# Kernel tuning notes

Measured on AMD Instinct MI355X. Metric: run time of the kernel, lower is better.

The kernel has to match this reference:

```python
import jax, jax.numpy as jnp
import numpy as np

# Model dims (match init_kwargs)
DIM = 1024
EXPAND = 2
D_INNER = DIM * EXPAND          # 2048
D_STATE = 16
D_CONV = 4
DT_RANK = max(16, DIM // 16)    # 64
BATCH = 2
SEQ = 1024
EPS_RMS = 1e-6


def setup_inputs() -> dict:
    key = jax.random.key(0)
    ks = jax.random.split(key, 10)
    def nrm(k, shape, scale=0.02):
        return jax.random.normal(k, shape, jnp.float32) * scale
    x = jax.random.normal(ks[0], (BATCH, SEQ, DIM), jnp.float32)
    W_in = nrm(ks[1], (2 * D_INNER, DIM))                      # in_proj, no bias
    W_conv = nrm(ks[2], (D_INNER, D_CONV), 0.1)                # depthwise conv weight (squeezed)
    b_conv = nrm(ks[3], (D_INNER,), 0.01)
    W_x = nrm(ks[4], (DT_RANK + 2 * D_STATE, D_INNER))         # x_proj, no bias
    dt_std = DT_RANK ** -0.5 * 0.1
    W_dt = jax.random.uniform(ks[5], (D_INNER, DT_RANK), jnp.float32, -dt_std, dt_std)
    b_dt = jax.random.uniform(ks[6], (D_INNER,), jnp.float32, 1e-3, 0.1)
    # HiPPO-style A init: A = arange(1..d_state) + small noise, A_log = log(A)
    A = jnp.arange(1, D_STATE + 1, dtype=jnp.float32)[None, :] + 0.01 * jax.random.normal(ks[7], (D_INNER, D_STATE), jnp.float32)
    A_log = jnp.log(A + 1e-8)
    D = jnp.ones((D_INNER,), jnp.float32) * 0.1
    rms_w = jnp.ones((D_INNER,), jnp.float32)                  # RMSNorm weight
    W_out = nrm(ks[8], (DIM, D_INNER))                         # out_proj, no bias
    return dict(x=x, W_in=W_in, W_conv=W_conv, b_conv=b_conv, W_x=W_x,
                W_dt=W_dt, b_dt=b_dt, A_log=A_log, D=D, rms_w=rms_w, W_out=W_out)


def _ssm_forward(x, W_in, W_conv, b_conv, W_x, W_dt, b_dt, A_log, D, rms_w, W_out):
    b, s, _ = x.shape
    # input projection -> [b, s, 2*d_inner], split into x branch and gate z
    xz = jnp.einsum('bsd,ed->bse', x, W_in)
    x_in, z = jnp.split(xz, 2, axis=-1)
    # depthwise causal conv1d (torch pads d_conv-1 both sides then slices to seq_len == left pad)
    xpad = jnp.pad(x_in, ((0, 0), (D_CONV - 1, 0), (0, 0)))
    xc = b_conv
    for k in range(D_CONV):
        xc = xc + W_conv[:, k] * xpad[:, k:k + s, :]
    xc = jax.nn.silu(xc)                                       # [b, s, d_inner]
    # data-dependent SSM params
    dbl = jnp.einsum('bsd,ed->bse', xc, W_x)
    dt, Bm, Cm = jnp.split(dbl, [DT_RANK, DT_RANK + D_STATE], axis=-1)
    dt = jax.nn.softplus(jnp.einsum('bsr,dr->bsd', dt, W_dt) + b_dt) + 1e-4  # [b,s,d_inner]
    A = -jnp.exp(A_log)                                        # [d_inner, d_state]
    # discretize: dA = exp(clip(dt*A)), dB*u
    dA = jnp.exp(jnp.clip(dt[..., None] * A, -10.0, 10.0))     # [b,s,d,n]
    dBu = dt[..., None] * Bm[:, :, None, :] * xc[..., None]    # [b,s,d,n]
    # selective scan: h_t = dA_t * h_{t-1} + dB_t * u_t ; y_t = <h_t, C_t>
    def step(h, inp):
        dA_t, dBu_t, C_t = inp
        h = dA_t * h + dBu_t
        y = jnp.einsum('bdn,bn->bd', h, C_t)
        return h, y
    h0 = jnp.zeros((b, D_INNER, D_STATE), x.dtype)
    _, ys = jax.lax.scan(step, h0,
                         (jnp.moveaxis(dA, 1, 0), jnp.moveaxis(dBu, 1, 0), jnp.moveaxis(Cm, 1, 0)))
    y = jnp.moveaxis(ys, 0, 1) + xc * D                        # skip connection u*D
    # gate, RMSNorm (eps=1e-6), out projection (dropout is identity in eval)
    y = y * jax.nn.silu(z)
    y = y * jax.lax.rsqrt(jnp.mean(y * y, axis=-1, keepdims=True) + EPS_RMS) * rms_w
    return jnp.einsum('bse,de->bsd', y, W_out)


def reference(x, W_in, W_conv, b_conv, W_x, W_dt, b_dt, A_log, D, rms_w, W_out):
    return _ssm_forward(x, W_in, W_conv, b_conv, W_x, W_dt, b_dt, A_log, D, rms_w, W_out)
```

## Files before the change

kernel.cpp:

```cpp
#include <hip/hip_runtime.h>
#include <hip/hip_bf16.h>

#define D_MODEL 1024
#define D_INNER 2048
#define D_STATE 16
#define D_CONVK 4
#define DT_RANK 64
#define BATCH   2
#define SEQ     1024
#define NROWS   (BATCH*SEQ)

#define NCHUNK  32
#define CHUNK   (SEQ/NCHUNK)

#define XZ_OFF  0
#define XZ_SZ   (NROWS*2*D_INNER)
#define XC_OFF  (XZ_OFF + XZ_SZ)
#define XC_SZ   (NROWS*D_INNER)
#define DBL_OFF (XC_OFF + XC_SZ)
#define DBL_SZ  (NROWS*96)
#define DT_OFF  (DBL_OFF + DBL_SZ)
#define DT_SZ   (NROWS*D_INNER)
#define YG_OFF  (DT_OFF + DT_SZ)
#define YG_SZ   (NROWS*D_INNER)

__device__ __forceinline__ float& plh_at(float* xz, int i) {
  return xz[((size_t)(i >> 11)) * (2 * D_INNER) + (i & (D_INNER - 1))];
}

typedef unsigned short ushort_t;
typedef __attribute__((ext_vector_type(8))) short  bf16x8;
typedef __attribute__((ext_vector_type(4))) float  f32x4;

__device__ __forceinline__ ushort_t f2bf(float f) {
  unsigned u = __float_as_uint(f);
  unsigned r = (u + 0x7fffu + ((u >> 16) & 1u)) >> 16;
  return (ushort_t)r;
}

__device__ __forceinline__ void gld_lds16(const ushort_t* g, ushort_t* l) {
  __builtin_amdgcn_global_load_lds(
      (const __attribute__((address_space(1))) unsigned int*)(const void*)g,
      (__attribute__((address_space(3))) unsigned int*)(void*)l,
      16, 0, 0);
}

__global__ __launch_bounds__(256) void f32_to_bf16_kernel(
    const float* __restrict__ src, ushort_t* __restrict__ dst, int n4)
{
  const int i = blockIdx.x * 256 + threadIdx.x;
  if (i >= n4) return;
  const float4 v = ((const float4*)src)[i];
  ushort4 o;
  o.x = f2bf(v.x); o.y = f2bf(v.y); o.z = f2bf(v.z); o.w = f2bf(v.w);
  ((ushort4*)dst)[i] = o;
}

__global__ __launch_bounds__(256) void gemm_bf16_nt(
    const ushort_t* __restrict__ A, int lda,
    const ushort_t* __restrict__ B, int ldb,
    float* __restrict__ C, int ldc,
    int M, int N, int K)
{
  __shared__ __attribute__((aligned(16))) ushort_t As[128 * 32];
  __shared__ __attribute__((aligned(16))) ushort_t Bs[128 * 32];

  const int tid  = threadIdx.x;
  const int wid  = tid >> 6;
  const int lane = tid & 63;
  const int wm   = wid >> 1;
  const int wn   = wid & 1;
  const int lm   = lane & 15;
  const int lk   = lane >> 4;
  const int bm   = blockIdx.y * 128;
  const int bn   = blockIdx.x * 128;

  const int srow = lane >> 2;
  const int scol = (lane & 3) * 8;

  f32x4 acc[4][4];
#pragma unroll
  for (int i = 0; i < 4; ++i)
#pragma unroll
    for (int j = 0; j < 4; ++j) acc[i][j] = (f32x4){0.f, 0.f, 0.f, 0.f};

  for (int k0 = 0; k0 < K; k0 += 32) {
    __syncthreads();
#pragma unroll
    for (int issue = 0; issue < 2; ++issue) {
      const int r = wid * 32 + issue * 16;
      gld_lds16(A + (size_t)(bm + r + srow) * lda + k0 + scol, &As[r * 32]);
      gld_lds16(B + (size_t)(bn + r + srow) * ldb + k0 + scol, &Bs[r * 32]);
    }
    __syncthreads();

    bf16x8 af[4], bf[4];
#pragma unroll
    for (int mi = 0; mi < 4; ++mi)
      af[mi] = *(const bf16x8*)&As[(wm * 64 + mi * 16 + lm) * 32 + lk * 8];
#pragma unroll
    for (int ni = 0; ni < 4; ++ni)
      bf[ni] = *(const bf16x8*)&Bs[(wn * 64 + ni * 16 + lm) * 32 + lk * 8];
#pragma unroll
    for (int mi = 0; mi < 4; ++mi)
#pragma unroll
      for (int ni = 0; ni < 4; ++ni)
        acc[mi][ni] = __builtin_amdgcn_mfma_f32_16x16x32_bf16(
            af[mi], bf[ni], acc[mi][ni], 0, 0, 0);
  }

#pragma unroll
  for (int mi = 0; mi < 4; ++mi) {
#pragma unroll
    for (int ni = 0; ni < 4; ++ni) {
      const f32x4 v = acc[mi][ni];
      const int row0 = bm + wm * 64 + mi * 16 + lk * 4;
      const int col  = bn + wn * 64 + ni * 16 + lm;
#pragma unroll
      for (int r = 0; r < 4; ++r)
        C[(size_t)(row0 + r) * ldc + col] = v[r];
    }
  }
}

#define XP_NS 16
#define XP_KC (D_INNER / XP_NS)
#define XP_BK 16

__global__ __launch_bounds__(256) void xproj_part_kernel(
    const float* __restrict__ A,
    const float* __restrict__ B,
    float* __restrict__ part)
{
  __shared__ float As[XP_BK][64 + 4];
  __shared__ float Bs[XP_BK][96 + 4];

  const int tid = threadIdx.x;
  const int bm = blockIdx.x * 64;
  const int kbase = blockIdx.y * XP_KC;
  const int tm = tid >> 4;
  const int tn = tid & 15;

  float acc[4][6];
#pragma unroll
  for (int i = 0; i < 4; ++i)
#pragma unroll
    for (int j = 0; j < 6; ++j) acc[i][j] = 0.f;

  for (int k0 = kbase; k0 < kbase + XP_KC; k0 += XP_BK) {
    {
      const int row = tid >> 2, kc = (tid & 3) * 4;
      const float4 v = *(const float4*)(A + (size_t)(bm + row) * D_INNER + k0 + kc);
      As[kc + 0][row] = v.x; As[kc + 1][row] = v.y;
      As[kc + 2][row] = v.z; As[kc + 3][row] = v.w;
    }
    for (int idx = tid; idx < 96 * 4; idx += 256) {
      const int row = idx >> 2, kc = (idx & 3) * 4;
      const float4 v = *(const float4*)(B + (size_t)row * D_INNER + k0 + kc);
      Bs[kc + 0][row] = v.x; Bs[kc + 1][row] = v.y;
      Bs[kc + 2][row] = v.z; Bs[kc + 3][row] = v.w;
    }
    __syncthreads();

#pragma unroll
    for (int kk = 0; kk < XP_BK; ++kk) {
      float a[4], b[6];
#pragma unroll
      for (int i = 0; i < 4; ++i) a[i] = As[kk][tm * 4 + i];
#pragma unroll
      for (int j = 0; j < 6; ++j) b[j] = Bs[kk][tn * 6 + j];
#pragma unroll
      for (int i = 0; i < 4; ++i)
#pragma unroll
        for (int j = 0; j < 6; ++j)
          acc[i][j] = fmaf(a[i], b[j], acc[i][j]);
    }
    __syncthreads();
  }

  float* p = part + (size_t)blockIdx.y * (NROWS * 96);
#pragma unroll
  for (int i = 0; i < 4; ++i) {
    const int gm = bm + tm * 4 + i;
#pragma unroll
    for (int j = 0; j < 6; ++j)
      p[(size_t)gm * 96 + tn * 6 + j] = acc[i][j];
  }
}

__global__ __launch_bounds__(256) void xproj_reduce_kernel(
    const float* __restrict__ part, float* __restrict__ dbl)
{
  const int i = blockIdx.x * 256 + threadIdx.x;
  const float4* p4 = (const float4*)part;
  float4 s = p4[i];
#pragma unroll
  for (int ks = 1; ks < XP_NS; ++ks) {
    const float4 v = p4[(size_t)ks * (NROWS * 96 / 4) + i];
    s.x += v.x; s.y += v.y; s.z += v.z; s.w += v.w;
  }
  ((float4*)dbl)[i] = s;
}

__global__ __launch_bounds__(256) void dtproj_kernel(
    const float* __restrict__ A,
    const float* __restrict__ B,
    const float* __restrict__ b_dt,
    float* __restrict__ C)
{
  __shared__ float As[16][128 + 4];
  __shared__ float Bs[16][128 + 4];

  const int tid = threadIdx.x;
  const int bm = blockIdx.y * 128;
  const int bn = blockIdx.x * 128;
  const int tm = tid >> 4;
  const int tn = tid & 15;

  float acc[8][8];
#pragma unroll
  for (int i = 0; i < 8; ++i)
#pragma unroll
    for (int j = 0; j < 8; ++j) acc[i][j] = 0.f;

  for (int k0 = 0; k0 < DT_RANK; k0 += 16) {
    for (int idx = tid; idx < 512; idx += 256) {
      const int row = idx >> 2, kc = (idx & 3) * 4;
      {
        const float4 v = *(const float4*)(A + (size_t)(bm + row) * 96 + k0 + kc);
        As[kc + 0][row] = v.x; As[kc + 1][row] = v.y;
        As[kc + 2][row] = v.z; As[kc + 3][row] = v.w;
      }
      {
        const float4 v = *(const float4*)(B + (size_t)(bn + row) * DT_RANK + k0 + kc);
        Bs[kc + 0][row] = v.x; Bs[kc + 1][row] = v.y;
        Bs[kc + 2][row] = v.z; Bs[kc + 3][row] = v.w;
      }
    }
    __syncthreads();

#pragma unroll
    for (int kk = 0; kk < 16; ++kk) {
      const float4 a0 = *(const float4*)&As[kk][tm * 8];
      const float4 a1 = *(const float4*)&As[kk][tm * 8 + 4];
      const float4 b0 = *(const float4*)&Bs[kk][tn * 8];
      const float4 b1 = *(const float4*)&Bs[kk][tn * 8 + 4];
      const float a[8] = {a0.x,a0.y,a0.z,a0.w,a1.x,a1.y,a1.z,a1.w};
      const float b[8] = {b0.x,b0.y,b0.z,b0.w,b1.x,b1.y,b1.z,b1.w};
#pragma unroll
      for (int i = 0; i < 8; ++i)
#pragma unroll
        for (int j = 0; j < 8; ++j)
          acc[i][j] = fmaf(a[i], b[j], acc[i][j]);
    }
    __syncthreads();
  }

  const int gn0 = bn + tn * 8;
  float bv[8];
#pragma unroll
  for (int j = 0; j < 8; ++j) bv[j] = b_dt[gn0 + j];
#pragma unroll
  for (int i = 0; i < 8; ++i) {
    const int gm = bm + tm * 8 + i;
    float o[8];
#pragma unroll
    for (int j = 0; j < 8; ++j) {
      const float v = acc[i][j] + bv[j];
      const float sp = (v > 20.f) ? v : log1pf(__expf(v));
      o[j] = sp + 1e-4f;
    }
    *(float4*)(C + (size_t)gm * D_INNER + gn0)     = make_float4(o[0], o[1], o[2], o[3]);
    *(float4*)(C + (size_t)gm * D_INNER + gn0 + 4) = make_float4(o[4], o[5], o[6], o[7]);
  }
}

__global__ __launch_bounds__(256) void conv_silu_kernel(
    const float* __restrict__ xz, const float* __restrict__ Wc,
    const float* __restrict__ bc, float* __restrict__ xc)
{
  const int idx = blockIdx.x * 256 + threadIdx.x;
  const int d = idx & (D_INNER - 1);
  const int m = idx >> 11;
  const int s = m & (SEQ - 1);
  const int mb = m - s;
  float acc = bc[d];
#pragma unroll
  for (int k = 0; k < D_CONVK; ++k) {
    const int t = s + k - (D_CONVK - 1);
    if (t >= 0)
      acc = fmaf(Wc[d * D_CONVK + k], xz[(size_t)(mb + t) * (2 * D_INNER) + d], acc);
  }
  xc[idx] = acc / (1.f + __expf(-acc));
}

__global__ __launch_bounds__(256) void scanA_kernel(
    const float* __restrict__ dtv, const float* __restrict__ xc,
    const float* __restrict__ dbl, const float* __restrict__ A_log,
    float* __restrict__ Pbuf, float* __restrict__ Lbuf)
{
  __shared__ float sB[CHUNK][16];

  const int tid = threadIdx.x;
  const int d = blockIdx.x * 256 + tid;
  const int chunk = blockIdx.y;
  const int b = blockIdx.z;
  const int rowbase = b * SEQ + chunk * CHUNK;

  for (int idx = tid; idx < CHUNK * 16; idx += 256) {
    const int i = idx >> 4, n = idx & 15;
    sB[i][n] = dbl[(size_t)(rowbase + i) * 96 + 64 + n];
  }

  float A_d[16];
#pragma unroll
  for (int j = 0; j < 4; ++j) {
    const float4 va = *(const float4*)&A_log[d * D_STATE + j * 4];
    A_d[j * 4 + 0] = -__expf(va.x);
    A_d[j * 4 + 1] = -__expf(va.y);
    A_d[j * 4 + 2] = -__expf(va.z);
    A_d[j * 4 + 3] = -__expf(va.w);
  }
  __syncthreads();

  float h[16], P[16];
#pragma unroll
  for (int n = 0; n < 16; ++n) { h[n] = 0.f; P[n] = 1.f; }

  for (int i = 0; i < CHUNK; ++i) {
    const size_t off = (size_t)(rowbase + i) * D_INNER + d;
    const float dt_v = dtv[off];
    const float dtxc = dt_v * xc[off];
    const float4 B0 = *(const float4*)&sB[i][0];
    const float4 B1 = *(const float4*)&sB[i][4];
    const float4 B2 = *(const float4*)&sB[i][8];
    const float4 B3 = *(const float4*)&sB[i][12];
    const float Bv[16] = {B0.x,B0.y,B0.z,B0.w, B1.x,B1.y,B1.z,B1.w,
                          B2.x,B2.y,B2.z,B2.w, B3.x,B3.y,B3.z,B3.w};
#pragma unroll
    for (int n = 0; n < 16; ++n) {
      float t = dt_v * A_d[n];
      t = fminf(fmaxf(t, -10.f), 10.f);
      const float dA = __expf(t);
      h[n] = fmaf(dA, h[n], dtxc * Bv[n]);
      P[n] *= dA;
    }
  }

  const size_t base = ((size_t)(chunk * BATCH + b) * 16) * D_INNER + d;
#pragma unroll
  for (int n = 0; n < 16; ++n) {
    Pbuf[base + (size_t)n * D_INNER] = P[n];
    Lbuf[base + (size_t)n * D_INNER] = h[n];
  }
}

__global__ __launch_bounds__(256) void scanB_kernel(
    const float* __restrict__ Pbuf, const float* __restrict__ Lbuf,
    float* __restrict__ xzp)
{
  const int t = blockIdx.x * 256 + threadIdx.x;
  const int d = t & (D_INNER - 1);
  const int n = (t >> 11) & 15;
  const int b = t >> 15;
  float hs = 0.f;
#pragma unroll
  for (int c = 0; c < NCHUNK; ++c) {
    const int idx = ((c * BATCH + b) * 16 + n) * D_INNER + d;
    plh_at(xzp, idx) = hs;
    hs = fmaf(Pbuf[idx], hs, Lbuf[idx]);
  }
}

__global__ __launch_bounds__(256) void scanC_kernel(
    const float* __restrict__ dtv, const float* __restrict__ xc,
    const float* __restrict__ dbl, const float* __restrict__ A_log,
    const float* __restrict__ Dp,  float* __restrict__ xzp,
    float* __restrict__ yg)
{
  __shared__ float sBC[CHUNK][32];

  const int tid = threadIdx.x;
  const int d = blockIdx.x * 256 + tid;
  const int chunk = blockIdx.y;
  const int b = blockIdx.z;
  const int rowbase = b * SEQ + chunk * CHUNK;

  for (int idx = tid; idx < CHUNK * 32; idx += 256) {
    const int i = idx >> 5, j = idx & 31;
    sBC[i][j] = dbl[(size_t)(rowbase + i) * 96 + 64 + j];
  }

  float A_d[16];
#pragma unroll
  for (int j = 0; j < 4; ++j) {
    const float4 va = *(const float4*)&A_log[d * D_STATE + j * 4];
    A_d[j * 4 + 0] = -__expf(va.x);
    A_d[j * 4 + 1] = -__expf(va.y);
    A_d[j * 4 + 2] = -__expf(va.z);
    A_d[j * 4 + 3] = -__expf(va.w);
  }
  const float Dd = Dp[d];
  __syncthreads();

  float h[16];
  {
    const int hbase = ((chunk * BATCH + b) * 16) * D_INNER + d;
#pragma unroll
    for (int n = 0; n < 16; ++n) h[n] = plh_at(xzp, hbase + n * D_INNER);
  }

  for (int i = 0; i < CHUNK; ++i) {
    const int m = rowbase + i;
    const size_t off = (size_t)m * D_INNER + d;
    const float dt_v = dtv[off];
    const float xc_v = xc[off];
    const float dtxc = dt_v * xc_v;
    const float4 B0 = *(const float4*)&sBC[i][0];
    const float4 B1 = *(const float4*)&sBC[i][4];
    const float4 B2 = *(const float4*)&sBC[i][8];
    const float4 B3 = *(const float4*)&sBC[i][12];
    const float4 C0 = *(const float4*)&sBC[i][16];
    const float4 C1 = *(const float4*)&sBC[i][20];
    const float4 C2 = *(const float4*)&sBC[i][24];
    const float4 C3 = *(const float4*)&sBC[i][28];
    const float Bv[16] = {B0.x,B0.y,B0.z,B0.w, B1.x,B1.y,B1.z,B1.w,
                          B2.x,B2.y,B2.z,B2.w, B3.x,B3.y,B3.z,B3.w};
    const float Cv[16] = {C0.x,C0.y,C0.z,C0.w, C1.x,C1.y,C1.z,C1.w,
                          C2.x,C2.y,C2.z,C2.w, C3.x,C3.y,C3.z,C3.w};
    float y = 0.f;
#pragma unroll
    for (int n = 0; n < 16; ++n) {
      float t = dt_v * A_d[n];
      t = fminf(fmaxf(t, -10.f), 10.f);
      const float dA = __expf(t);
      h[n] = fmaf(dA, h[n], dtxc * Bv[n]);
      y = fmaf(h[n], Cv[n], y);
    }
    const float zv = xzp[(size_t)m * (2 * D_INNER) + D_INNER + d];
    const float sil = zv / (1.f + __expf(-zv));
    yg[off] = (y + xc_v * Dd) * sil;
  }
}

__global__ __launch_bounds__(256) void rms_bf16_kernel(
    const float* __restrict__ yg, const float* __restrict__ rms_w,
    ushort_t* __restrict__ ygb)
{
  const int m = blockIdx.x;
  const float* row = yg + (size_t)m * D_INNER;
  const int e0 = threadIdx.x * 8;
  float4 v0 = *(const float4*)&row[e0];
  float4 v1 = *(const float4*)&row[e0 + 4];
  float ss = v0.x*v0.x + v0.y*v0.y + v0.z*v0.z + v0.w*v0.w
           + v1.x*v1.x + v1.y*v1.y + v1.z*v1.z + v1.w*v1.w;
#pragma unroll
  for (int off = 32; off > 0; off >>= 1) ss += __shfl_down(ss, off);
  __shared__ float wsum[4];
  const int lane = threadIdx.x & 63, wid = threadIdx.x >> 6;
  if (lane == 0) wsum[wid] = ss;
  __syncthreads();
  const float total = wsum[0] + wsum[1] + wsum[2] + wsum[3];
  const float scale = rsqrtf(total / (float)D_INNER + 1e-6f);
  const float4 w0 = *(const float4*)&rms_w[e0];
  const float4 w1 = *(const float4*)&rms_w[e0 + 4];
  ushort4 o0, o1;
  o0.x = f2bf(v0.x * scale * w0.x); o0.y = f2bf(v0.y * scale * w0.y);
  o0.z = f2bf(v0.z * scale * w0.z); o0.w = f2bf(v0.w * scale * w0.w);
  o1.x = f2bf(v1.x * scale * w1.x); o1.y = f2bf(v1.y * scale * w1.y);
  o1.z = f2bf(v1.z * scale * w1.z); o1.w = f2bf(v1.w * scale * w1.w);
  *(ushort4*)&ygb[(size_t)m * D_INNER + e0]     = o0;
  *(ushort4*)&ygb[(size_t)m * D_INNER + e0 + 4] = o1;
}

extern "C" void kernel_launch(void* const* d_in, const int* in_sizes, int n_in,
                              void* d_out, int out_size, void* d_ws, size_t ws_size,
                              hipStream_t stream) {
  const float* x      = (const float*)d_in[0];
  const float* W_in   = (const float*)d_in[1];
  const float* W_conv = (const float*)d_in[2];
  const float* b_conv = (const float*)d_in[3];
  const float* W_x    = (const float*)d_in[4];
  const float* W_dt   = (const float*)d_in[5];
  const float* b_dt   = (const float*)d_in[6];
  const float* A_log  = (const float*)d_in[7];
  const float* Dp     = (const float*)d_in[8];
  const float* rms_w  = (const float*)d_in[9];
  const float* W_out  = (const float*)d_in[10];
  float* out = (float*)d_out;
  float* ws  = (float*)d_ws;

  float* xz  = ws + XZ_OFF;
  float* xc  = ws + XC_OFF;
  float* dbl = ws + DBL_OFF;
  float* dt  = ws + DT_OFF;
  float* yg  = ws + YG_OFF;

  ushort_t* xb      = (ushort_t*)(ws + YG_OFF);
  ushort_t* W_in_b  = (ushort_t*)(ws + YG_OFF + 1024 * 1024);
  float*    xpart   = ws + DT_OFF;
  float*    Pbuf    = ws + YG_OFF;
  float*    Lbuf    = ws + YG_OFF + 2 * 1024 * 1024;
  ushort_t* ygb     = (ushort_t*)(ws + DT_OFF);
  ushort_t* W_out_b = (ushort_t*)(ws + DT_OFF + 2 * 1024 * 1024);

  f32_to_bf16_kernel<<<(NROWS * D_MODEL / 4 + 255) / 256, 256, 0, stream>>>(x, xb, NROWS * D_MODEL / 4);
  f32_to_bf16_kernel<<<(2 * D_INNER * D_MODEL / 4 + 255) / 256, 256, 0, stream>>>(W_in, W_in_b, 2 * D_INNER * D_MODEL / 4);

  {
    dim3 g((2 * D_INNER) / 128, NROWS / 128);
    gemm_bf16_nt<<<g, 256, 0, stream>>>(xb, D_MODEL, W_in_b, D_MODEL, xz, 2 * D_INNER,
                                        NROWS, 2 * D_INNER, D_MODEL);
  }
  conv_silu_kernel<<<(NROWS * D_INNER) / 256, 256, 0, stream>>>(xz, W_conv, b_conv, xc);
  {
    dim3 g(NROWS / 64, XP_NS);
    xproj_part_kernel<<<g, 256, 0, stream>>>(xc, W_x, xpart);
    xproj_reduce_kernel<<<(NROWS * 96 / 4) / 256, 256, 0, stream>>>(xpart, dbl);
  }
  {
    dim3 g(D_INNER / 128, NROWS / 128);
    dtproj_kernel<<<g, 256, 0, stream>>>(dbl, W_dt, b_dt, dt);
  }
  {
    dim3 gAC(D_INNER / 256, NCHUNK, BATCH);
    scanA_kernel<<<gAC, 256, 0, stream>>>(dt, xc, dbl, A_log, Pbuf, Lbuf);
    scanB_kernel<<<(BATCH * D_INNER * 16) / 256, 256, 0, stream>>>(Pbuf, Lbuf, xz);
    scanC_kernel<<<gAC, 256, 0, stream>>>(dt, xc, dbl, A_log, Dp, xz, yg);
  }
  rms_bf16_kernel<<<NROWS, 256, 0, stream>>>(yg, rms_w, ygb);
  f32_to_bf16_kernel<<<(D_MODEL * D_INNER / 4 + 255) / 256, 256, 0, stream>>>(W_out, W_out_b, D_MODEL * D_INNER / 4);
  {
    dim3 g(D_MODEL / 128, NROWS / 128);
    gemm_bf16_nt<<<g, 256, 0, stream>>>(ygb, D_INNER, W_out_b, D_INNER, out, D_MODEL,
                                        NROWS, D_MODEL, D_INNER);
  }
}
```

Before: 321.7 us.

## Use single-wave 64x64 GEMM tiles with swizzled LDS and split-K for out_proj

Replaces the 256-thread 128x128 bf16 MFMA GEMM with a one-wave 64x64 tile kernel. It XOR-swizzles the LDS layout to avoid bank conflicts and adds a split-K=2 path for the output projection, followed by a reduction kernel. The aim is more blocks and better CU occupancy for these modest-size GEMMs. The trade-off is less data reuse per block, an extra partial-sum buffer written into the xc workspace region, and an extra reduce launch.

```diff
diff --git a/kernel.cpp b/kernel.cpp
--- a/kernel.cpp
+++ b/kernel.cpp
@@ -56,27 +56,25 @@
   ((ushort4*)dst)[i] = o;
 }
 
-__global__ __launch_bounds__(256) void gemm_bf16_nt(
+__global__ __launch_bounds__(64, 4) void gemm_bf16_wave(
     const ushort_t* __restrict__ A, int lda,
     const ushort_t* __restrict__ B, int ldb,
-    float* __restrict__ C, int ldc,
-    int M, int N, int K)
-{
-  __shared__ __attribute__((aligned(16))) ushort_t As[128 * 32];
-  __shared__ __attribute__((aligned(16))) ushort_t Bs[128 * 32];
-
-  const int tid  = threadIdx.x;
-  const int wid  = tid >> 6;
-  const int lane = tid & 63;
-  const int wm   = wid >> 1;
-  const int wn   = wid & 1;
-  const int lm   = lane & 15;
-  const int lk   = lane >> 4;
-  const int bm   = blockIdx.y * 128;
-  const int bn   = blockIdx.x * 128;
-
-  const int srow = lane >> 2;
-  const int scol = (lane & 3) * 8;
+    float* __restrict__ C, int ldc, int klen)
+{
+  __shared__ __attribute__((aligned(16))) ushort_t As[64 * 32];
+  __shared__ __attribute__((aligned(16))) ushort_t Bs[64 * 32];
+
+  const int l  = threadIdx.x;
+  const int lm = l & 15;
+  const int lk = l >> 4;
+  const int bn = blockIdx.x * 64;
+  const int bm = blockIdx.y * 64;
+  const int kbase = blockIdx.z * klen;
+  float* Cz = C + (size_t)blockIdx.z * (size_t)gridDim.y * 64 * ldc;
+
+  const int srow  = l >> 2;
+  const int scol  = ((l & 3) ^ ((l >> 3) & 3)) * 8;
+  const int rslot = (lk ^ ((lm >> 1) & 3)) * 8;
 
   f32x4 acc[4][4];
 #pragma unroll
@@ -84,23 +82,23 @@
 #pragma unroll
     for (int j = 0; j < 4; ++j) acc[i][j] = (f32x4){0.f, 0.f, 0.f, 0.f};
 
-  for (int k0 = 0; k0 < K; k0 += 32) {
+  for (int k0 = kbase; k0 < kbase + klen; k0 += 32) {
     __syncthreads();
 #pragma unroll
-    for (int issue = 0; issue < 2; ++issue) {
-      const int r = wid * 32 + issue * 16;
-      gld_lds16(A + (size_t)(bm + r + srow) * lda + k0 + scol, &As[r * 32]);
-      gld_lds16(B + (size_t)(bn + r + srow) * ldb + k0 + scol, &Bs[r * 32]);
-    }
+    for (int i = 0; i < 4; ++i)
+      gld_lds16(A + (size_t)(bm + i * 16 + srow) * lda + k0 + scol, &As[i * 16 * 32]);
+#pragma unroll
+    for (int i = 0; i < 4; ++i)
+      gld_lds16(B + (size_t)(bn + i * 16 + srow) * ldb + k0 + scol, &Bs[i * 16 * 32]);
     __syncthreads();
 
     bf16x8 af[4], bf[4];
 #pragma unroll
     for (int mi = 0; mi < 4; ++mi)
-      af[mi] = *(const bf16x8*)&As[(wm * 64 + mi * 16 + lm) * 32 + lk * 8];
+      af[mi] = *(const bf16x8*)&As[(mi * 16 + lm) * 32 + rslot];
 #pragma unroll
     for (int ni = 0; ni < 4; ++ni)
-      bf[ni] = *(const bf16x8*)&Bs[(wn * 64 + ni * 16 + lm) * 32 + lk * 8];
+      bf[ni] = *(const bf16x8*)&Bs[(ni * 16 + lm) * 32 + rslot];
 #pragma unroll
     for (int mi = 0; mi < 4; ++mi)
 #pragma unroll
@@ -114,13 +112,22 @@
 #pragma unroll
     for (int ni = 0; ni < 4; ++ni) {
       const f32x4 v = acc[mi][ni];
-      const int row0 = bm + wm * 64 + mi * 16 + lk * 4;
-      const int col  = bn + wn * 64 + ni * 16 + lm;
+      const int row0 = bm + mi * 16 + lk * 4;
+      const int col  = bn + ni * 16 + lm;
 #pragma unroll
       for (int r = 0; r < 4; ++r)
-        C[(size_t)(row0 + r) * ldc + col] = v[r];
-    }
-  }
+        Cz[(size_t)(row0 + r) * ldc + col] = v[r];
+    }
+  }
+}
+
+__global__ __launch_bounds__(256) void splitk2_reduce_kernel(
+    const float* __restrict__ part, float* __restrict__ out)
+{
+  const int i = blockIdx.x * 256 + threadIdx.x;
+  const float4 a = ((const float4*)part)[i];
+  const float4 b = ((const float4*)part)[i + (NROWS * D_MODEL / 4)];
+  ((float4*)out)[i] = make_float4(a.x + b.x, a.y + b.y, a.z + b.z, a.w + b.w);
 }
 
 #define XP_NS 16
@@ -503,14 +510,14 @@
   float*    Lbuf    = ws + YG_OFF + 2 * 1024 * 1024;
   ushort_t* ygb     = (ushort_t*)(ws + DT_OFF);
   ushort_t* W_out_b = (ushort_t*)(ws + DT_OFF + 2 * 1024 * 1024);
+  float*    opart   = ws + XC_OFF;
 
   f32_to_bf16_kernel<<<(NROWS * D_MODEL / 4 + 255) / 256, 256, 0, stream>>>(x, xb, NROWS * D_MODEL / 4);
   f32_to_bf16_kernel<<<(2 * D_INNER * D_MODEL / 4 + 255) / 256, 256, 0, stream>>>(W_in, W_in_b, 2 * D_INNER * D_MODEL / 4);
 
   {
-    dim3 g((2 * D_INNER) / 128, NROWS / 128);
-    gemm_bf16_nt<<<g, 256, 0, stream>>>(xb, D_MODEL, W_in_b, D_MODEL, xz, 2 * D_INNER,
-                                        NROWS, 2 * D_INNER, D_MODEL);
+    dim3 g((2 * D_INNER) / 64, NROWS / 64, 1);
+    gemm_bf16_wave<<<g, 64, 0, stream>>>(xb, D_MODEL, W_in_b, D_MODEL, xz, 2 * D_INNER, D_MODEL);
   }
   conv_silu_kernel<<<(NROWS * D_INNER) / 256, 256, 0, stream>>>(xz, W_conv, b_conv, xc);
   {
@@ -531,8 +538,8 @@
   rms_bf16_kernel<<<NROWS, 256, 0, stream>>>(yg, rms_w, ygb);
   f32_to_bf16_kernel<<<(D_MODEL * D_INNER / 4 + 255) / 256, 256, 0, stream>>>(W_out, W_out_b, D_MODEL * D_INNER / 4);
   {
-    dim3 g(D_MODEL / 128, NROWS / 128);
-    gemm_bf16_nt<<<g, 256, 0, stream>>>(ygb, D_INNER, W_out_b, D_INNER, out, D_MODEL,
-                                        NROWS, D_MODEL, D_INNER);
-  }
-}
+    dim3 g(D_MODEL / 64, NROWS / 64, 2);
+    gemm_bf16_wave<<<g, 64, 0, stream>>>(ygb, D_INNER, W_out_b, D_INNER, opart, D_MODEL, D_INNER / 2);
+    splitk2_reduce_kernel<<<(NROWS * D_MODEL / 4) / 256, 256, 0, stream>>>(opart, out);
+  }
+}
```

New measurement: 303.3 us. 5.7% less time.
